# Performance work log

Hardware: AMD Instinct MI355X
Metric: run time of the kernel (lower is better)

The kernel has to match this reference:

```python
import jax, jax.numpy as jnp
from jax import lax
import numpy as np

INPUT = 80
H1 = 100
H2 = 50


def _lstm_layer(x, Wih, Whh, bih, bhh):
    """PyTorch-semantics single-layer LSTM, batch_first.
    x: [B,T,I]; Wih: [4H,I]; Whh: [4H,H]; biases: [4H]. Gate order: i,f,g,o.
    Returns full hidden sequence [B,T,H]."""
    B, T, _ = x.shape
    H = Whh.shape[1]
    # precompute input projections for all timesteps (one big GEMM)
    pre = jnp.einsum('bti,gi->tbg', x, Wih) + (bih + bhh)  # [T,B,4H]

    def step(carry, p):
        h, c = carry
        gates = p + h @ Whh.T  # [B,4H]
        i, f, g, o = jnp.split(gates, 4, axis=-1)
        i = jax.nn.sigmoid(i)
        f = jax.nn.sigmoid(f)
        g = jnp.tanh(g)
        o = jax.nn.sigmoid(o)
        c = f * c + i * g
        h = o * jnp.tanh(c)
        return (h, c), h

    h0 = jnp.zeros((B, H), x.dtype)
    (_, _), hs = lax.scan(step, (h0, h0), pre)  # hs: [T,B,H]
    return jnp.transpose(hs, (1, 0, 2))  # [B,T,H]


def setup_inputs() -> dict:
    key = jax.random.key(0)
    ks = jax.random.split(key, 9)
    B, T = 1024, 512
    s1 = 1.0 / np.sqrt(H1)
    s2 = 1.0 / np.sqrt(H2)
    return {
        'x': jax.random.normal(ks[0], (B, T, INPUT), dtype=jnp.float32),
        'Wih1': jax.random.uniform(ks[1], (4 * H1, INPUT), jnp.float32, -s1, s1),
        'Whh1': jax.random.uniform(ks[2], (4 * H1, H1), jnp.float32, -s1, s1),
        'bih1': jax.random.uniform(ks[3], (4 * H1,), jnp.float32, -s1, s1),
        'bhh1': jax.random.uniform(ks[4], (4 * H1,), jnp.float32, -s1, s1),
        'Wih2': jax.random.uniform(ks[5], (4 * H2, H1), jnp.float32, -s2, s2),
        'Whh2': jax.random.uniform(ks[6], (4 * H2, H2), jnp.float32, -s2, s2),
        'bih2': jax.random.uniform(ks[7], (4 * H2,), jnp.float32, -s2, s2),
        'bhh2': jax.random.uniform(ks[8], (4 * H2,), jnp.float32, -s2, s2),
    }


def reference(x, Wih1, Whh1, bih1, bhh1, Wih2, Whh2, bih2, bhh2):
    # Dropout layers are identity in eval mode.
    h1 = _lstm_layer(x, Wih1, Whh1, bih1, bhh1)   # [B,T,100]
    h2 = _lstm_layer(h1, Wih2, Whh2, bih2, bhh2)  # [B,T,50]
    return h2[:, -1, :]                            # [B,50]
```

## Files before the change

### kernel.cpp

```cpp
#include <hip/hip_runtime.h>

#define BT 1024
#define TT 512

__device__ __forceinline__ float sig_(float x) { return 1.f / (1.f + __expf(-x)); }
__device__ __forceinline__ float th_(float x)  { return 1.f - 2.f / (1.f + __expf(2.f * x)); }

template <int K, int KPAD, int N, bool XMODE>
__global__ __launch_bounds__(256) void gemm_pre(
    const float* __restrict__ A, const float* __restrict__ W,
    const float* __restrict__ bih, const float* __restrict__ bhh,
    float* __restrict__ out, int t0)
{
    __shared__ float As[128][KPAD];
    __shared__ __align__(16) float Bs[K][64];
    const int tid = threadIdx.x;
    const int n0 = blockIdx.x * 64;
    const int Rbase = blockIdx.y * 128;
    const int NQ = K / 4;

    for (int ii = tid; ii < 128 * NQ; ii += 256) {
        int r = ii / NQ, q = ii % NQ;
        const float* src;
        if (XMODE) {
            int b  = (blockIdx.y & 7) * 128 + r;
            int tl = blockIdx.y >> 3;
            src = A + ((size_t)b * TT + (t0 + tl)) * K;
        } else {
            src = A + (size_t)(Rbase + r) * K;
        }
        float4 v = *(const float4*)(src + q * 4);
        As[r][q * 4 + 0] = v.x; As[r][q * 4 + 1] = v.y;
        As[r][q * 4 + 2] = v.z; As[r][q * 4 + 3] = v.w;
    }
    for (int ii = tid; ii < 64 * NQ; ii += 256) {
        int n = ii & 63, kq = ii >> 6;
        float4 v = make_float4(0.f, 0.f, 0.f, 0.f);
        if (n0 + n < N) v = *(const float4*)(W + (size_t)(n0 + n) * K + kq * 4);
        Bs[kq * 4 + 0][n] = v.x; Bs[kq * 4 + 1][n] = v.y;
        Bs[kq * 4 + 2][n] = v.z; Bs[kq * 4 + 3][n] = v.w;
    }
    __syncthreads();

    const int tx = tid & 15, ty = tid >> 4;
    float acc[8][4];
#pragma unroll
    for (int i = 0; i < 8; i++)
#pragma unroll
        for (int jj = 0; jj < 4; jj++) acc[i][jj] = 0.f;

#pragma unroll 4
    for (int k = 0; k < K; k++) {
        float4 bv = *(const float4*)&Bs[k][tx * 4];
#pragma unroll
        for (int i = 0; i < 8; i++) {
            float a = As[ty * 8 + i][k];
            acc[i][0] += a * bv.x; acc[i][1] += a * bv.y;
            acc[i][2] += a * bv.z; acc[i][3] += a * bv.w;
        }
    }
    int n = n0 + tx * 4;
    if (n < N) {
        float4 bias;
        bias.x = bih[n] + bhh[n];     bias.y = bih[n + 1] + bhh[n + 1];
        bias.z = bih[n + 2] + bhh[n + 2]; bias.w = bih[n + 3] + bhh[n + 3];
#pragma unroll
        for (int i = 0; i < 8; i++) {
            size_t R = (size_t)Rbase + ty * 8 + i;
            float4 o;
            o.x = acc[i][0] + bias.x; o.y = acc[i][1] + bias.y;
            o.z = acc[i][2] + bias.z; o.w = acc[i][3] + bias.w;
            *(float4*)(out + R * N + n) = o;
        }
    }
}

__global__ __launch_bounds__(512, 4) void rec1(
    const float* __restrict__ pre,
    const float* __restrict__ Whh,
    float* __restrict__ hseq,
    float* __restrict__ cst,
    int Tc, int first)
{
    __shared__ __align__(16) float hs[2][100];
    __shared__ __align__(16) float pres[2][800];
    __shared__ float gbuf[5 * 4 * 2 * 100];
    const int tid = threadIdx.x;
    const int b0 = blockIdx.x * 2;

    const bool comp = tid < 500;
    const int j  = tid % 100;
    const int kq = tid / 100;

    float4 w[4][5];
    if (comp) {
#pragma unroll
        for (int g = 0; g < 4; g++) {
            const float4* W4 = (const float4*)(Whh + (size_t)(g * 100 + j) * 100);
#pragma unroll
            for (int q = 0; q < 5; q++) w[g][q] = W4[kq * 5 + q];
        }
    }

    const bool upd = tid < 200;
    const int ub = tid / 100, uj = tid % 100;
    float c = 0.f;
    if (upd) {
        float h = 0.f;
        if (!first) {
            h = hseq[((size_t)(Tc - 1) * BT + b0 + ub) * 100 + uj];
            c = cst[(size_t)(b0 + ub) * 100 + uj];
        }
        hs[ub][uj] = h;
        ((float4*)pres[0])[tid] = ((const float4*)(pre + (size_t)b0 * 400))[tid];
    }
    __syncthreads();

    int cur = 0;
    for (int t = 0; t < Tc; t++) {
        int tn = (t + 1 < Tc) ? (t + 1) : t;
        float4 pf0;
        if (upd)
            pf0 = ((const float4*)(pre + (size_t)tn * BT * 400 + (size_t)b0 * 400))[tid];

        if (comp) {
            float acc[4][2];
#pragma unroll
            for (int g = 0; g < 4; g++) { acc[g][0] = 0.f; acc[g][1] = 0.f; }
            const float4* h0 = (const float4*)hs[0];
            const float4* h1 = (const float4*)hs[1];
#pragma unroll
            for (int q = 0; q < 5; q++) {
                int f = kq * 5 + q;
                float4 v0 = h0[f], v1 = h1[f];
#pragma unroll
                for (int g = 0; g < 4; g++) {
                    float4 wq = w[g][q];
                    acc[g][0] = fmaf(wq.x, v0.x, acc[g][0]);
                    acc[g][0] = fmaf(wq.y, v0.y, acc[g][0]);
                    acc[g][0] = fmaf(wq.z, v0.z, acc[g][0]);
                    acc[g][0] = fmaf(wq.w, v0.w, acc[g][0]);
                    acc[g][1] = fmaf(wq.x, v1.x, acc[g][1]);
                    acc[g][1] = fmaf(wq.y, v1.y, acc[g][1]);
                    acc[g][1] = fmaf(wq.z, v1.z, acc[g][1]);
                    acc[g][1] = fmaf(wq.w, v1.w, acc[g][1]);
                }
            }
#pragma unroll
            for (int g = 0; g < 4; g++) {
                gbuf[((kq * 4 + g) * 2 + 0) * 100 + j] = acc[g][0];
                gbuf[((kq * 4 + g) * 2 + 1) * 100 + j] = acc[g][1];
            }
        }
        __syncthreads();

        if (upd) {
            const float* pb = pres[cur];
            float s0 = 0.f, s1 = 0.f, s2 = 0.f, s3 = 0.f;
#pragma unroll
            for (int q = 0; q < 5; q++) {
                int base = q * 800;
                s0 += gbuf[base + (0 * 2 + ub) * 100 + uj];
                s1 += gbuf[base + (1 * 2 + ub) * 100 + uj];
                s2 += gbuf[base + (2 * 2 + ub) * 100 + uj];
                s3 += gbuf[base + (3 * 2 + ub) * 100 + uj];
            }
            float xi = s0 + pb[ub * 400 + uj];
            float xf = s1 + pb[ub * 400 + 100 + uj];
            float xg = s2 + pb[ub * 400 + 200 + uj];
            float xo = s3 + pb[ub * 400 + 300 + uj];
            float ii = sig_(xi), ff = sig_(xf), gg = th_(xg), oo = sig_(xo);
            c = ff * c + ii * gg;
            float h = oo * th_(c);
            hs[ub][uj] = h;
            hseq[((size_t)t * BT + b0 + ub) * 100 + uj] = h;
            ((float4*)pres[cur ^ 1])[tid] = pf0;
        }
        __syncthreads();
        cur ^= 1;
    }
    if (upd) cst[(size_t)(b0 + ub) * 100 + uj] = c;
}

__global__ __launch_bounds__(256, 4) void rec2(
    const float* __restrict__ pre2,
    const float* __restrict__ Whh,
    float* __restrict__ cst, float* __restrict__ hst,
    float* __restrict__ out,
    int Tc, int first)
{
    __shared__ __align__(16) float hs[2][50];
    __shared__ __align__(16) float pres[2][400];
    __shared__ float gbuf[5 * 4 * 2 * 50];
    const int tid = threadIdx.x;
    const int b0 = blockIdx.x * 2;

    const bool comp = tid < 250;
    const int j  = tid % 50;
    const int kq = tid / 50;

    float2 w[4][5];
    if (comp) {
#pragma unroll
        for (int g = 0; g < 4; g++) {
            const float2* W2 = (const float2*)(Whh + (size_t)(g * 50 + j) * 50);
#pragma unroll
            for (int q = 0; q < 5; q++) w[g][q] = W2[kq * 5 + q];
        }
    }

    const bool upd = tid < 100;
    const int ub = tid / 50, uj = tid % 50;
    float c = 0.f, hlast = 0.f;
    if (upd) {
        float h = 0.f;
        if (!first) {
            h = hst[(size_t)(b0 + ub) * 50 + uj];
            c = cst[(size_t)(b0 + ub) * 50 + uj];
        }
        hs[ub][uj] = h;
        hlast = h;
        ((float4*)pres[0])[tid] = ((const float4*)(pre2 + (size_t)b0 * 200))[tid];
    }
    __syncthreads();

    int cur = 0;
    for (int t = 0; t < Tc; t++) {
        int tn = (t + 1 < Tc) ? (t + 1) : t;
        float4 pf0;
        if (upd)
            pf0 = ((const float4*)(pre2 + (size_t)tn * BT * 200 + (size_t)b0 * 200))[tid];

        if (comp) {
            float acc[4][2];
#pragma unroll
            for (int g = 0; g < 4; g++) { acc[g][0] = 0.f; acc[g][1] = 0.f; }
            const float2* hA = (const float2*)hs[0];
            const float2* hB = (const float2*)hs[1];
#pragma unroll
            for (int q = 0; q < 5; q++) {
                int f = kq * 5 + q;
                float2 v0 = hA[f], v1 = hB[f];
#pragma unroll
                for (int g = 0; g < 4; g++) {
                    float2 wq = w[g][q];
                    acc[g][0] = fmaf(wq.x, v0.x, acc[g][0]);
                    acc[g][0] = fmaf(wq.y, v0.y, acc[g][0]);
                    acc[g][1] = fmaf(wq.x, v1.x, acc[g][1]);
                    acc[g][1] = fmaf(wq.y, v1.y, acc[g][1]);
                }
            }
#pragma unroll
            for (int g = 0; g < 4; g++) {
                gbuf[((kq * 4 + g) * 2 + 0) * 50 + j] = acc[g][0];
                gbuf[((kq * 4 + g) * 2 + 1) * 50 + j] = acc[g][1];
            }
        }
        __syncthreads();

        if (upd) {
            const float* pb = pres[cur];
            float s0 = 0.f, s1 = 0.f, s2 = 0.f, s3 = 0.f;
#pragma unroll
            for (int q = 0; q < 5; q++) {
                int base = q * 400;
                s0 += gbuf[base + (0 * 2 + ub) * 50 + uj];
                s1 += gbuf[base + (1 * 2 + ub) * 50 + uj];
                s2 += gbuf[base + (2 * 2 + ub) * 50 + uj];
                s3 += gbuf[base + (3 * 2 + ub) * 50 + uj];
            }
            float xi = s0 + pb[ub * 200 + uj];
            float xf = s1 + pb[ub * 200 + 50 + uj];
            float xg = s2 + pb[ub * 200 + 100 + uj];
            float xo = s3 + pb[ub * 200 + 150 + uj];
            float ii = sig_(xi), ff = sig_(xf), gg = th_(xg), oo = sig_(xo);
            c = ff * c + ii * gg;
            float h = oo * th_(c);
            hs[ub][uj] = h;
            hlast = h;
            ((float4*)pres[cur ^ 1])[tid] = pf0;
        }
        __syncthreads();
        cur ^= 1;
    }
    if (upd) {
        cst[(size_t)(b0 + ub) * 50 + uj] = c;
        hst[(size_t)(b0 + ub) * 50 + uj] = hlast;
        out[(size_t)(b0 + ub) * 50 + uj] = hlast;
    }
}

extern "C" void kernel_launch(void* const* d_in, const int* in_sizes, int n_in,
                              void* d_out, int out_size, void* d_ws, size_t ws_size,
                              hipStream_t stream)
{
    const float* x    = (const float*)d_in[0];
    const float* Wih1 = (const float*)d_in[1];
    const float* Whh1 = (const float*)d_in[2];
    const float* bih1 = (const float*)d_in[3];
    const float* bhh1 = (const float*)d_in[4];
    const float* Wih2 = (const float*)d_in[5];
    const float* Whh2 = (const float*)d_in[6];
    const float* bih2 = (const float*)d_in[7];
    const float* bhh2 = (const float*)d_in[8];
    float* out = (float*)d_out;
    float* ws  = (float*)d_ws;

    int Tc = 64;
    auto need = [](int tc) -> size_t {
        return ((size_t)tc * 1024 * (400 + 100 + 200) +
                (size_t)1024 * 100 + (size_t)1024 * 50 * 2) * sizeof(float);
    };
    while (Tc > 1 && need(Tc) > ws_size) Tc >>= 1;

    float* pre1 = ws;
    float* h1s  = pre1 + (size_t)Tc * 1024 * 400;
    float* pre2 = h1s  + (size_t)Tc * 1024 * 100;
    float* c1   = pre2 + (size_t)Tc * 1024 * 200;
    float* c2   = c1 + 1024 * 100;
    float* h2st = c2 + 1024 * 50;

    const int nch = TT / Tc;
    for (int ch = 0; ch < nch; ch++) {
        int t0 = ch * Tc;
        gemm_pre<80, 81, 400, true ><<<dim3(7, Tc * 8), 256, 0, stream>>>(
            x, Wih1, bih1, bhh1, pre1, t0);
        rec1<<<dim3(512), dim3(512), 0, stream>>>(pre1, Whh1, h1s, c1, Tc, ch == 0 ? 1 : 0);
        gemm_pre<100, 101, 200, false><<<dim3(4, Tc * 8), 256, 0, stream>>>(
            h1s, Wih2, bih2, bhh2, pre2, 0);
        rec2<<<dim3(512), dim3(256), 0, stream>>>(pre2, Whh2, c2, h2st, out, Tc, ch == 0 ? 1 : 0);
    }
}
```

Baseline: 2.928 ms.

## Split pre-projection GEMM K into two LDS stages with vectorized A reads

The input-projection GEMM now loads and computes the K dimension in two halves, reusing smaller shared-memory tiles. This roughly halves LDS per block and raises occupancy, backed by a launch-bounds hint. The inner loop now reads A as float4 over four k values, and rows are interleaved (ty+16*i) to cut LDS instruction count. It adds an extra barrier and staging pass, and only the GEMM kernels change, not the recurrent kernels.

```diff
diff --git a/kernel.cpp b/kernel.cpp
--- a/kernel.cpp
+++ b/kernel.cpp
@@ -6,67 +6,108 @@
 __device__ __forceinline__ float sig_(float x) { return 1.f / (1.f + __expf(-x)); }
 __device__ __forceinline__ float th_(float x)  { return 1.f - 2.f / (1.f + __expf(2.f * x)); }
 
-template <int K, int KPAD, int N, bool XMODE>
-__global__ __launch_bounds__(256) void gemm_pre(
+template <int KS, int KPAD, int KH, int N, bool XMODE>
+__device__ __forceinline__ void gp_stage(
+    const float* __restrict__ A, const float* __restrict__ W,
+    float (&As)[128][KPAD], float (&Bs)[KPAD][64],
+    int tid, int n0, int by, int t0, int k0)
+{
+    constexpr int NQH = KH / 4;
+#pragma unroll
+    for (int ii = tid; ii < 128 * NQH; ii += 256) {
+        int r = ii / NQH, q = ii % NQH;
+        const float* src;
+        if (XMODE) {
+            int b  = (by & 7) * 128 + r;
+            int tl = by >> 3;
+            src = A + ((size_t)b * TT + (t0 + tl)) * KS;
+        } else {
+            src = A + (size_t)(by * 128 + r) * KS;
+        }
+        float4 v = *(const float4*)(src + k0 + q * 4);
+        As[r][q * 4 + 0] = v.x; As[r][q * 4 + 1] = v.y;
+        As[r][q * 4 + 2] = v.z; As[r][q * 4 + 3] = v.w;
+    }
+#pragma unroll
+    for (int ii = tid; ii < 64 * NQH; ii += 256) {
+        int n = ii & 63, kq = ii >> 6;
+        float4 v = make_float4(0.f, 0.f, 0.f, 0.f);
+        if (n0 + n < N) v = *(const float4*)(W + (size_t)(n0 + n) * KS + k0 + kq * 4);
+        Bs[kq * 4 + 0][n] = v.x; Bs[kq * 4 + 1][n] = v.y;
+        Bs[kq * 4 + 2][n] = v.z; Bs[kq * 4 + 3][n] = v.w;
+    }
+}
+
+template <int KPAD, int KH>
+__device__ __forceinline__ void gp_compute(
+    const float (&As)[128][KPAD], const float (&Bs)[KPAD][64],
+    float (&acc)[8][4], int tx, int ty)
+{
+    for (int kk = 0; kk < KH; kk += 4) {
+        float4 bv0 = *(const float4*)&Bs[kk + 0][tx * 4];
+        float4 bv1 = *(const float4*)&Bs[kk + 1][tx * 4];
+        float4 bv2 = *(const float4*)&Bs[kk + 2][tx * 4];
+        float4 bv3 = *(const float4*)&Bs[kk + 3][tx * 4];
+#pragma unroll
+        for (int i = 0; i < 8; i++) {
+            float4 av = *(const float4*)&As[ty + 16 * i][kk];
+            acc[i][0] = fmaf(av.x, bv0.x, acc[i][0]);
+            acc[i][0] = fmaf(av.y, bv1.x, acc[i][0]);
+            acc[i][0] = fmaf(av.z, bv2.x, acc[i][0]);
+            acc[i][0] = fmaf(av.w, bv3.x, acc[i][0]);
+            acc[i][1] = fmaf(av.x, bv0.y, acc[i][1]);
+            acc[i][1] = fmaf(av.y, bv1.y, acc[i][1]);
+            acc[i][1] = fmaf(av.z, bv2.y, acc[i][1]);
+            acc[i][1] = fmaf(av.w, bv3.y, acc[i][1]);
+            acc[i][2] = fmaf(av.x, bv0.z, acc[i][2]);
+            acc[i][2] = fmaf(av.y, bv1.z, acc[i][2]);
+            acc[i][2] = fmaf(av.z, bv2.z, acc[i][2]);
+            acc[i][2] = fmaf(av.w, bv3.z, acc[i][2]);
+            acc[i][3] = fmaf(av.x, bv0.w, acc[i][3]);
+            acc[i][3] = fmaf(av.y, bv1.w, acc[i][3]);
+            acc[i][3] = fmaf(av.z, bv2.w, acc[i][3]);
+            acc[i][3] = fmaf(av.w, bv3.w, acc[i][3]);
+        }
+    }
+}
+
+template <int KS, int KPAD, int KH0, int N, bool XMODE>
+__global__ __launch_bounds__(256, 4) void gemm_pre(
     const float* __restrict__ A, const float* __restrict__ W,
     const float* __restrict__ bih, const float* __restrict__ bhh,
     float* __restrict__ out, int t0)
 {
-    __shared__ float As[128][KPAD];
-    __shared__ __align__(16) float Bs[K][64];
+    constexpr int KH1 = KS - KH0;
+    __shared__ __align__(16) float As[128][KPAD];
+    __shared__ __align__(16) float Bs[KPAD][64];
     const int tid = threadIdx.x;
     const int n0 = blockIdx.x * 64;
-    const int Rbase = blockIdx.y * 128;
-    const int NQ = K / 4;
-
-    for (int ii = tid; ii < 128 * NQ; ii += 256) {
-        int r = ii / NQ, q = ii % NQ;
-        const float* src;
-        if (XMODE) {
-            int b  = (blockIdx.y & 7) * 128 + r;
-            int tl = blockIdx.y >> 3;
-            src = A + ((size_t)b * TT + (t0 + tl)) * K;
-        } else {
-            src = A + (size_t)(Rbase + r) * K;
-        }
-        float4 v = *(const float4*)(src + q * 4);
-        As[r][q * 4 + 0] = v.x; As[r][q * 4 + 1] = v.y;
-        As[r][q * 4 + 2] = v.z; As[r][q * 4 + 3] = v.w;
-    }
-    for (int ii = tid; ii < 64 * NQ; ii += 256) {
-        int n = ii & 63, kq = ii >> 6;
-        float4 v = make_float4(0.f, 0.f, 0.f, 0.f);
-        if (n0 + n < N) v = *(const float4*)(W + (size_t)(n0 + n) * K + kq * 4);
-        Bs[kq * 4 + 0][n] = v.x; Bs[kq * 4 + 1][n] = v.y;
-        Bs[kq * 4 + 2][n] = v.z; Bs[kq * 4 + 3][n] = v.w;
-    }
-    __syncthreads();
-
+    const int by = blockIdx.y;
+    const int Rbase = by * 128;
     const int tx = tid & 15, ty = tid >> 4;
+
     float acc[8][4];
 #pragma unroll
     for (int i = 0; i < 8; i++)
 #pragma unroll
-        for (int jj = 0; jj < 4; jj++) acc[i][jj] = 0.f;
-
-#pragma unroll 4
-    for (int k = 0; k < K; k++) {
-        float4 bv = *(const float4*)&Bs[k][tx * 4];
-#pragma unroll
-        for (int i = 0; i < 8; i++) {
-            float a = As[ty * 8 + i][k];
-            acc[i][0] += a * bv.x; acc[i][1] += a * bv.y;
-            acc[i][2] += a * bv.z; acc[i][3] += a * bv.w;
-        }
-    }
+        for (int j = 0; j < 4; j++) acc[i][j] = 0.f;
+
+    gp_stage<KS, KPAD, KH0, N, XMODE>(A, W, As, Bs, tid, n0, by, t0, 0);
+    __syncthreads();
+    gp_compute<KPAD, KH0>(As, Bs, acc, tx, ty);
+    __syncthreads();
+    gp_stage<KS, KPAD, KH1, N, XMODE>(A, W, As, Bs, tid, n0, by, t0, KH0);
+    __syncthreads();
+    gp_compute<KPAD, KH1>(As, Bs, acc, tx, ty);
+
     int n = n0 + tx * 4;
     if (n < N) {
         float4 bias;
-        bias.x = bih[n] + bhh[n];     bias.y = bih[n + 1] + bhh[n + 1];
+        bias.x = bih[n] + bhh[n];         bias.y = bih[n + 1] + bhh[n + 1];
         bias.z = bih[n + 2] + bhh[n + 2]; bias.w = bih[n + 3] + bhh[n + 3];
 #pragma unroll
         for (int i = 0; i < 8; i++) {
-            size_t R = (size_t)Rbase + ty * 8 + i;
+            size_t R = (size_t)Rbase + ty + 16 * i;
             float4 o;
             o.x = acc[i][0] + bias.x; o.y = acc[i][1] + bias.y;
             o.z = acc[i][2] + bias.z; o.w = acc[i][3] + bias.w;
@@ -323,10 +364,10 @@
     const int nch = TT / Tc;
     for (int ch = 0; ch < nch; ch++) {
         int t0 = ch * Tc;
-        gemm_pre<80, 81, 400, true ><<<dim3(7, Tc * 8), 256, 0, stream>>>(
+        gemm_pre<80, 40, 40, 400, true ><<<dim3(7, Tc * 8), 256, 0, stream>>>(
             x, Wih1, bih1, bhh1, pre1, t0);
         rec1<<<dim3(512), dim3(512), 0, stream>>>(pre1, Whh1, h1s, c1, Tc, ch == 0 ? 1 : 0);
-        gemm_pre<100, 101, 200, false><<<dim3(4, Tc * 8), 256, 0, stream>>>(
+        gemm_pre<100, 52, 52, 200, false><<<dim3(4, Tc * 8), 256, 0, stream>>>(
             h1s, Wih2, bih2, bhh2, pre2, 0);
         rec2<<<dim3(512), dim3(256), 0, stream>>>(pre2, Whh2, c2, h2st, out, Tc, ch == 0 ? 1 : 0);
     }
```

After: 2.580 ms. 11.9% less time.
